# Kernel tuning notes

Measured on AMD Instinct MI355X. Metric: run time of the kernel, lower is better.

Reference implementation:

```python
import jax, jax.numpy as jnp
import numpy as np

NH = 12
LEVEL = 4  # Lmin = 2**LEVEL = 16


def _build_sets(T, Lmin):
    l_list, r_list = [], []
    L = Lmin
    while L <= T:
        for i in range(T // L):
            l_list.append(i * L)
            r_list.append((i + 1) * L - 1)
        L *= 2
    return np.asarray(l_list, np.int32), np.asarray(r_list, np.int32)


def _get_slice(x_cum, l_idx, r_idx):
    # x_cum: [B,nh,T,hs]; returns inclusive range-sums x[l..r] via cumsum diffs
    r = x_cum[:, :, r_idx, :]
    l = x_cum[:, :, np.maximum(np.asarray(l_idx) - 1, 0), :]
    mask = (np.asarray(l_idx) >= 1).astype(x_cum.dtype)[None, None, :, None]
    return r - l * mask


def _get_slice_dyn(x_cum, l_idx, r_idx):
    # same but with traced/jnp indices (tail term)
    r = x_cum[:, :, r_idx, :]
    l = x_cum[:, :, jnp.maximum(l_idx - 1, 0), :]
    mask = (l_idx >= 1).astype(x_cum.dtype)[None, None, :, None]
    return r - l * mask


def setup_inputs() -> dict:
    key = jax.random.key(0)
    k0, k1, k2, k3 = jax.random.split(key, 4)
    B, T, C = 8, 2048, 768
    hs = C // NH
    s = 0.02
    return {
        "x": jax.random.normal(k0, (B, T, C), jnp.float32),
        "Wqkv": jax.random.normal(k1, (3 * C, C), jnp.float32) * s,
        "Wproj": jax.random.normal(k2, (C, C), jnp.float32) * s,
        "Wv": jax.random.normal(k3, (hs, hs * hs), jnp.float32) * s,
        "bv": jnp.zeros((hs,), jnp.float32),
    }


def reference(x, Wqkv, Wproj, Wv, bv):
    B, T, C = x.shape
    nh = NH
    hs = C // nh
    Lmin = 2 ** LEVEL
    scale = 1.0 / jnp.sqrt(jnp.asarray(hs, x.dtype))

    qkv = x @ Wqkv.T  # [B,T,3C]
    q, k, v0 = jnp.split(qkv, 3, axis=-1)
    q = q.reshape(B, T, nh, hs).transpose(0, 2, 1, 3)   # [B,nh,T,hs]
    k = k.reshape(B, T, nh, hs).transpose(0, 2, 1, 3)
    v0 = v0.reshape(B, T, nh, hs).transpose(0, 2, 1, 3)

    # v = v_proj(outer(k, v0).flatten)  == einsum with Wv reshaped [hs,hs,hs]
    Wv3 = Wv.reshape(hs, hs, hs)
    v = jnp.einsum('bhti,bhtj,eij->bhte', k, v0, Wv3) + bv

    k_cum = jnp.cumsum(k, axis=2)
    v_cum = jnp.cumsum(v, axis=2)

    l_idx, r_idx = _build_sets(T, Lmin)  # static dyadic sets
    K = _get_slice(k_cum, l_idx, r_idx)  # [B,nh,S,hs]
    V = _get_slice(v_cum, l_idx, r_idx)

    t_idx = jnp.arange(T)
    mask = t_idx[:, None] >= jnp.asarray(r_idx)[None, :]  # [T,S]
    logits = jnp.einsum('bhtd,bhsd->bhts', q, K) * scale
    logits = jnp.where(mask[None, None], logits, -jnp.inf)

    # tail: remainder within the current Lmin block
    l_tail = (t_idx // Lmin) * Lmin
    K_tail = _get_slice_dyn(k_cum, l_tail, t_idx)  # [B,nh,T,hs]
    V_tail = _get_slice_dyn(v_cum, l_tail, t_idx)
    tail_logits = jnp.sum(q * K_tail, axis=-1) * scale  # [B,nh,T]

    att = jax.nn.softmax(jnp.concatenate([logits, tail_logits[..., None]], axis=-1), axis=-1)
    out = jnp.einsum('bhts,bhsd->bhtd', att[..., :-1], V) + att[..., -1:] * V_tail
    out = out.transpose(0, 2, 1, 3).reshape(B, T, C)
    return out @ Wproj.T
```

## Files before the change

kernel.cpp:

```cpp
#include <hip/hip_runtime.h>


typedef float  f32x4  __attribute__((ext_vector_type(4)));
typedef _Float16 half8 __attribute__((ext_vector_type(8)));
typedef _Float16 half4 __attribute__((ext_vector_type(4)));

#define DEV __device__ __forceinline__
#define MFMA16(a, b, c) __builtin_amdgcn_mfma_f32_16x16x32_f16((a), (b), (c), 0, 0, 0)
#define GLOAD16(gp, lp)                                                  \
  __builtin_amdgcn_global_load_lds(                                      \
      (const __attribute__((address_space(1))) unsigned int*)(gp),       \
      (__attribute__((address_space(3))) unsigned int*)(lp), 16, 0, 0)

__global__ __launch_bounds__(256) void k_cast16(const float* __restrict__ in,
                                                _Float16* __restrict__ outh, int n4) {
  int i = blockIdx.x * 256 + threadIdx.x;
  if (i >= n4) return;
  f32x4 v = ((const f32x4*)in)[i];
  half4 o;
#pragma unroll
  for (int c = 0; c < 4; ++c) o[c] = (_Float16)v[c];
  ((half4*)outh)[i] = o;
}

__global__ __launch_bounds__(256) void k_castw(const float* __restrict__ Wqkv,
                                               const float* __restrict__ Wv,
                                               const float* __restrict__ Wproj,
                                               _Float16* __restrict__ wq,
                                               _Float16* __restrict__ wv,
                                               _Float16* __restrict__ wp) {
  int i = blockIdx.x * 256 + threadIdx.x;
  const float* src;
  _Float16* dst;
  int idx = i;
  if (idx < 442368) { src = Wqkv; dst = wq; }
  else if (idx < 442368 + 65536) { src = Wv; dst = wv; idx -= 442368; }
  else if (idx < 442368 + 65536 + 147456) { src = Wproj; dst = wp; idx -= 442368 + 65536; }
  else return;
  f32x4 v = ((const f32x4*)src)[idx];
  half4 o;
#pragma unroll
  for (int c = 0; c < 4; ++c) o[c] = (_Float16)v[c];
  ((half4*)dst)[idx] = o;
}

__global__ __launch_bounds__(256, 3) void k_gemm_qkv(
    const _Float16* __restrict__ A16, const _Float16* __restrict__ B16,
    _Float16* __restrict__ qo, _Float16* __restrict__ ko, _Float16* __restrict__ v0o) {
  __shared__ _Float16 sA[128][64], sB[128][64];
  const int K = 768;
  int tid = threadIdx.x, lane = tid & 63, wave = tid >> 6;
  int l15 = lane & 15, g = lane >> 4;
  int wr = wave >> 1, wc = wave & 1;
  int wg = (blockIdx.x & 7) * 288 + (blockIdx.x >> 3);
  int n0 = (wg % 18) * 128, m0 = (wg / 18) * 128;
  f32x4 acc[4][4];
#pragma unroll
  for (int a = 0; a < 4; ++a)
#pragma unroll
    for (int b = 0; b < 4; ++b) acc[a][b] = f32x4{0.f, 0.f, 0.f, 0.f};
  int rsel = lane >> 3;
  int csel = (lane & 7) ^ rsel;
  for (int k0 = 0; k0 < K; k0 += 64) {
#pragma unroll
    for (int r = 0; r < 4; ++r) {
      int row = wave * 32 + r * 8 + rsel;
      GLOAD16(&A16[(size_t)(m0 + row) * K + k0 + csel * 8], &sA[wave * 32 + r * 8][0]);
      GLOAD16(&B16[(size_t)(n0 + row) * K + k0 + csel * 8], &sB[wave * 32 + r * 8][0]);
    }
    __syncthreads();
#pragma unroll
    for (int kk = 0; kk < 2; ++kk) {
      int kc = kk * 4 + g;
      int cc = ((kc ^ (l15 & 7)) << 3);
      half8 af[4], bf[4];
#pragma unroll
      for (int mf = 0; mf < 4; ++mf) af[mf] = *(const half8*)&sA[wr * 64 + mf * 16 + l15][cc];
#pragma unroll
      for (int nf = 0; nf < 4; ++nf) bf[nf] = *(const half8*)&sB[wc * 64 + nf * 16 + l15][cc];
#pragma unroll
      for (int mf = 0; mf < 4; ++mf)
#pragma unroll
        for (int nf = 0; nf < 4; ++nf)
          acc[mf][nf] = MFMA16(af[mf], bf[nf], acc[mf][nf]);
    }
    __syncthreads();
  }
  int sec = n0 / 768;
  int nb = n0 - sec * 768;
#pragma unroll
  for (int mf = 0; mf < 4; ++mf)
#pragma unroll
    for (int nf = 0; nf < 4; ++nf)
#pragma unroll
      for (int r = 0; r < 4; ++r) {
        int m = m0 + wr * 64 + mf * 16 + (g << 2) + r;
        int n = nb + wc * 64 + nf * 16 + l15;
        int b = m >> 11, t = m & 2047;
        int h = n >> 6, d = n & 63;
        size_t idx = (((size_t)b * 12 + h) * 2048 + t) * 64 + d;
        _Float16 val = (_Float16)acc[mf][nf][r];
        if (sec == 0) qo[idx] = val;
        else if (sec == 1) ko[idx] = val;
        else v0o[idx] = val;
      }
}

__global__ __launch_bounds__(256, 3) void k_veins(
    const _Float16* __restrict__ kh, const _Float16* __restrict__ v0g,
    const _Float16* __restrict__ Wvh, const float* __restrict__ bv,
    _Float16* __restrict__ vout) {
  __shared__ _Float16 ks[256][72];
  __shared__ _Float16 sB[2][64][64];
  int tid = threadIdx.x, lane = tid & 63, wave = tid >> 6;
  int l15 = lane & 15, g = lane >> 4, g8 = g << 3;
  size_t row0 = (size_t)blockIdx.x * 256;

  int srow_lo = wave * 8 + (lane >> 3);
  int scsrc = (lane & 7) ^ (lane >> 3);
  auto STAGE = [&](int b, int i) {
#pragma unroll
    for (int h = 0; h < 2; ++h) {
      GLOAD16(&Wvh[(size_t)(h * 32 + srow_lo) * 4096 + i * 64 + (scsrc << 3)],
              ((_Float16*)sB) + (size_t)b * 4096 + (h * 256 + wave * 64) * 8);
    }
  };

#pragma unroll
  for (int r = 0; r < 8; ++r) {
    int row = (tid >> 3) + r * 32;
    int c8 = (tid & 7) << 3;
    *(half8*)&ks[row][c8] = *(const half8*)&kh[(row0 + row) * 64 + c8];
  }
  half8 v0r[4][2];
#pragma unroll
  for (int mf = 0; mf < 4; ++mf) {
    size_t rb = (row0 + wave * 64 + mf * 16 + l15) * 64;
#pragma unroll
    for (int kk = 0; kk < 2; ++kk)
      v0r[mf][kk] = *(const half8*)&v0g[rb + kk * 32 + g8];
  }
  f32x4 acc[4][4];
#pragma unroll
  for (int a = 0; a < 4; ++a)
#pragma unroll
    for (int b = 0; b < 4; ++b) acc[a][b] = f32x4{0.f, 0.f, 0.f, 0.f};

  STAGE(0, 0);
  __syncthreads();
  int r0 = wave * 64 + l15;
  for (int i8 = 0; i8 < 8; ++i8) {
    half8 kr0 = *(const half8*)&ks[r0][i8 * 8];
    half8 kr1 = *(const half8*)&ks[r0 + 16][i8 * 8];
    half8 kr2 = *(const half8*)&ks[r0 + 32][i8 * 8];
    half8 kr3 = *(const half8*)&ks[r0 + 48][i8 * 8];
#pragma unroll
    for (int ii = 0; ii < 8; ++ii) {
      int i = i8 * 8 + ii;
      int cur = i & 1;
      if (i < 63) STAGE(cur ^ 1, i + 1);
      half8 b0[4], b1[4];
#pragma unroll
      for (int nf = 0; nf < 4; ++nf) {
        b0[nf] = *(const half8*)&sB[cur][nf * 16 + l15][((g ^ (l15 & 7)) << 3)];
        b1[nf] = *(const half8*)&sB[cur][nf * 16 + l15][(((4 + g) ^ (l15 & 7)) << 3)];
      }
      _Float16 kv0 = kr0[ii], kv1 = kr1[ii], kv2 = kr2[ii], kv3 = kr3[ii];
      {
        half8 a0 = v0r[0][0] * kv0, a1 = v0r[1][0] * kv1;
        half8 a2 = v0r[2][0] * kv2, a3 = v0r[3][0] * kv3;
#pragma unroll
        for (int nf = 0; nf < 4; ++nf) {
          acc[0][nf] = MFMA16(a0, b0[nf], acc[0][nf]);
          acc[1][nf] = MFMA16(a1, b0[nf], acc[1][nf]);
          acc[2][nf] = MFMA16(a2, b0[nf], acc[2][nf]);
          acc[3][nf] = MFMA16(a3, b0[nf], acc[3][nf]);
        }
      }
      {
        half8 a0 = v0r[0][1] * kv0, a1 = v0r[1][1] * kv1;
        half8 a2 = v0r[2][1] * kv2, a3 = v0r[3][1] * kv3;
#pragma unroll
        for (int nf = 0; nf < 4; ++nf) {
          acc[0][nf] = MFMA16(a0, b1[nf], acc[0][nf]);
          acc[1][nf] = MFMA16(a1, b1[nf], acc[1][nf]);
          acc[2][nf] = MFMA16(a2, b1[nf], acc[2][nf]);
          acc[3][nf] = MFMA16(a3, b1[nf], acc[3][nf]);
        }
      }
      __syncthreads();
    }
  }
#pragma unroll
  for (int mf = 0; mf < 4; ++mf)
#pragma unroll
    for (int nf = 0; nf < 4; ++nf) {
      int e = (nf << 4) + l15;
      float bve = bv[e];
#pragma unroll
      for (int r = 0; r < 4; ++r) {
        int row = wave * 64 + mf * 16 + (g << 2) + r;
        vout[(row0 + row) * 64 + e] = (_Float16)(acc[mf][nf][r] + bve);
      }
    }
}

__global__ __launch_bounds__(256) void k_segments(
    const _Float16* __restrict__ kmat, const _Float16* __restrict__ vmat,
    _Float16* __restrict__ Ks, _Float16* __restrict__ Vt) {
  __shared__ float Ls[255][64];
  int s = blockIdx.x;
  int bh = (s & 7) * 12 + (s >> 3);
  int tid = threadIdx.x;
  size_t bh2048 = (size_t)bh * 2048;
  for (int task = tid; task < 8192; task += 256) {
    int seg = task >> 6, d = task & 63;
    const _Float16* p = kmat + (bh2048 + seg * 16) * 64 + d;
    float sm = 0.f;
#pragma unroll
    for (int u = 0; u < 16; ++u) sm += (float)p[u * 64];
    Ls[seg][d] = sm;
  }
  __syncthreads();
  {
    int bprev = 0, bcur = 128, cnt = 64;
    for (int lev = 1; lev < 8; ++lev) {
      for (int task = tid; task < cnt * 64; task += 256) {
        int i = task >> 6, d = task & 63;
        Ls[bcur + i][d] = Ls[bprev + 2 * i][d] + Ls[bprev + 2 * i + 1][d];
      }
      __syncthreads();
      bprev = bcur; bcur += cnt; cnt >>= 1;
    }
  }
  for (int task = tid; task < 16384; task += 256) {
    int seg = task >> 6;
    float v = (seg < 255) ? Ls[seg][task & 63] : 0.f;
    Ks[(size_t)bh * 16384 + task] = (_Float16)v;
  }
  __syncthreads();
  for (int task = tid; task < 8192; task += 256) {
    int seg = task >> 6, d = task & 63;
    const _Float16* p = vmat + (bh2048 + seg * 16) * 64 + d;
    float sm = 0.f;
#pragma unroll
    for (int u = 0; u < 16; ++u) sm += (float)p[u * 64];
    Ls[seg][d] = sm;
  }
  __syncthreads();
  {
    int bprev = 0, bcur = 128, cnt = 64;
    for (int lev = 1; lev < 8; ++lev) {
      for (int task = tid; task < cnt * 64; task += 256) {
        int i = task >> 6, d = task & 63;
        Ls[bcur + i][d] = Ls[bprev + 2 * i][d] + Ls[bprev + 2 * i + 1][d];
      }
      __syncthreads();
      bprev = bcur; bcur += cnt; cnt >>= 1;
    }
  }
  for (int task = tid; task < 16384; task += 256) {
    int d = task >> 8, seg = task & 255;
    float v = (seg < 255) ? Ls[seg][d] : 0.f;
    Vt[(size_t)bh * 16384 + task] = (_Float16)v;
  }
}

__global__ __launch_bounds__(256) void k_tails(
    const _Float16* __restrict__ km, const _Float16* __restrict__ vm,
    _Float16* __restrict__ tKg, _Float16* __restrict__ tVt) {
  int B = blockIdx.x;
  int bh = (B & 7) * 12 + (B >> 6);
  int seg16 = ((B >> 3) & 7) * 16;
  int wave = threadIdx.x >> 6, lane = threadIdx.x & 63;
  for (int task = wave; task < 32; task += 4) {
    int blk = seg16 + (task >> 1);
    size_t base = ((size_t)bh * 2048 + blk * 16) * 64 + lane;
    if (!(task & 1)) {
      float ka = 0.f;
      _Float16* o = tKg + (((size_t)bh * 128 + blk) * 16) * 64 + lane;
#pragma unroll
      for (int t = 0; t < 16; ++t) {
        ka += (float)km[base + t * 64];
        o[t * 64] = (_Float16)ka;
      }
    } else {
      float va = 0.f;
      half8 lo = {}, hi = {};
#pragma unroll
      for (int t = 0; t < 8; ++t) {
        va += (float)vm[base + t * 64];
        lo[t] = (_Float16)va;
      }
#pragma unroll
      for (int t = 0; t < 8; ++t) {
        va += (float)vm[base + (t + 8) * 64];
        hi[t] = (_Float16)va;
      }
      _Float16* o = tVt + (((size_t)bh * 128 + blk) * 64 + lane) * 16;
      ((half8*)o)[0] = lo;
      ((half8*)o)[1] = hi;
    }
  }
}

__global__ __launch_bounds__(256, 3) void k_attn2(
    const _Float16* __restrict__ qm,
    const _Float16* __restrict__ tKg, const _Float16* __restrict__ tVt,
    const _Float16* __restrict__ Ks, const _Float16* __restrict__ Vt,
    _Float16* __restrict__ outp) {
  __shared__ __align__(16) _Float16 P[4][16][280];
  __shared__ __align__(16) _Float16 sKs[2][32][64];
  __shared__ __align__(16) _Float16 sVt[2][64][32];
  int tid = threadIdx.x, lane = tid & 63, wave = tid >> 6;
  int orig = blockIdx.y * 32 + blockIdx.x;
  int wg = (orig & 7) * 384 + (orig >> 3);
  int tile = wg & 31, bh = wg >> 5;
  int t0 = tile * 64, tw0 = t0 + wave * 16;
  int blkw = tile * 4 + wave;
  size_t bh2048 = (size_t)bh * 2048;
  int l15 = lane & 15, g = lane >> 4, g8 = g << 3;

  const _Float16* KsB = Ks + (size_t)bh * 16384;
  const _Float16* VB = Vt + (size_t)bh * 16384;

  auto STAGE_K = [&](int buf, int c) {
    GLOAD16(KsB + (size_t)(c * 32 + wave * 8 + (lane >> 3)) * 64 +
                (((lane & 7) ^ ((lane >> 3) & 7)) << 3),
            &sKs[buf][wave * 8][0]);
  };
  auto STAGE_VT = [&](int buf, int c) {
    GLOAD16(VB + (size_t)(wave * 16 + (lane >> 2)) * 256 + c * 32 +
                (((lane & 3) ^ ((lane >> 2) & 3)) << 3),
            &sVt[buf][wave * 16][0]);
  };

  half8 qf0, qf1, t0f, t1f;
  {
    const _Float16* qp = qm + (bh2048 + tw0 + l15) * 64 + g8;
    qf0 = *(const half8*)qp;
    qf1 = *(const half8*)(qp + 32);
    const _Float16* tp = tKg + (((size_t)bh * 128 + blkw) * 16 + l15) * 64 + g8;
    t0f = *(const half8*)tp;
    t1f = *(const half8*)(tp + 32);
  }
  STAGE_K(0, 0);

  unsigned mA = 0, mE = 0;
#pragma unroll
  for (int nf = 0; nf < 16; ++nf) {
    int seg = nf * 16 + l15;
    if (seg < 255) {
      int m = 256 - seg;
      int cl = 32 - __clz(m - 1);
      int lev = 8 - cl;
      int rdx = (seg - (256 - (256 >> lev)) + 1) * (16 << lev) - 1;
      if (rdx < tw0) mA |= 1u << nf;
      else if (rdx == tw0 + 15) mE |= 1u << nf;
    }
  }

  f32x4 acc[17];
#pragma unroll
  for (int i = 0; i < 17; ++i) acc[i] = f32x4{0.f, 0.f, 0.f, 0.f};

  __syncthreads();
#pragma unroll
  for (int c = 0; c < 8; ++c) {
    if (c < 7) STAGE_K((c + 1) & 1, c + 1);
    int bs = c & 1;
#pragma unroll
    for (int p = 0; p < 2; ++p) {
      int row = p * 16 + l15;
      half8 b0 = *(const half8*)&sKs[bs][row][(g ^ (l15 & 7)) << 3];
      half8 b1 = *(const half8*)&sKs[bs][row][((g + 4) ^ (l15 & 7)) << 3];
      acc[2 * c + p] = MFMA16(qf0, b0, acc[2 * c + p]);
      acc[2 * c + p] = MFMA16(qf1, b1, acc[2 * c + p]);
    }
    __syncthreads();
  }
  acc[16] = MFMA16(qf0, t0f, acc[16]);
  acc[16] = MFMA16(qf1, t1f, acc[16]);

  STAGE_VT(0, 0);
  STAGE_VT(1, 1);

  const float c2 = 0.125f * 1.44269504f;
  float mx[4], sm[4], et[4];
#pragma unroll
  for (int r = 0; r < 4; ++r) {
    int tr = g * 4 + r;
    mx[r] = (l15 == tr) ? acc[16][r] * c2 : -3.0e38f;
  }
#pragma unroll
  for (int nf = 0; nf < 16; ++nf) {
    bool bA = (mA >> nf) & 1, bE = (mE >> nf) & 1;
#pragma unroll
    for (int r = 0; r < 4; ++r) {
      bool u = bA || (bE && g == 3 && r == 3);
      if (u) mx[r] = fmaxf(mx[r], acc[nf][r] * c2);
    }
  }
#pragma unroll
  for (int off = 1; off < 16; off <<= 1)
#pragma unroll
    for (int r = 0; r < 4; ++r) mx[r] = fmaxf(mx[r], __shfl_xor(mx[r], off));
#pragma unroll
  for (int r = 0; r < 4; ++r) {
    int tr = g * 4 + r;
    et[r] = (l15 == tr) ? exp2f(acc[16][r] * c2 - mx[r]) : 0.f;
    sm[r] = et[r];
  }
#pragma unroll
  for (int nf = 0; nf < 16; ++nf) {
    bool bA = (mA >> nf) & 1, bE = (mE >> nf) & 1;
#pragma unroll
    for (int r = 0; r < 4; ++r) {
      bool u = bA || (bE && g == 3 && r == 3);
      float e = u ? exp2f(acc[nf][r] * c2 - mx[r]) : 0.f;
      acc[nf][r] = e;
      sm[r] += e;
    }
  }
#pragma unroll
  for (int off = 1; off < 16; off <<= 1)
#pragma unroll
    for (int r = 0; r < 4; ++r) sm[r] += __shfl_xor(sm[r], off);
  float inv[4];
#pragma unroll
  for (int r = 0; r < 4; ++r) inv[r] = 1.f / sm[r];

  {
    half4 z4 = {};
    *(half4*)&P[wave][lane >> 2][256 + (lane & 3) * 4] = z4;
  }
#pragma unroll
  for (int nf = 0; nf < 16; ++nf)
#pragma unroll
    for (int r = 0; r < 4; ++r)
      P[wave][g * 4 + r][nf * 16 + l15] = (_Float16)acc[nf][r];
#pragma unroll
  for (int r = 0; r < 4; ++r)
    if (l15 == g * 4 + r) P[wave][l15][256 + l15] = (_Float16)et[r];

  f32x4 oa[4];
#pragma unroll
  for (int i = 0; i < 4; ++i) oa[i] = f32x4{0.f, 0.f, 0.f, 0.f};
  __syncthreads();
#pragma unroll
  for (int c = 0; c < 8; ++c) {
    int bs = c & 1;
    half8 pa = *(const half8*)&P[wave][l15][c * 32 + g8];
#pragma unroll
    for (int n2 = 0; n2 < 4; ++n2) {
      half8 vb = *(const half8*)&sVt[bs][n2 * 16 + l15][(g ^ (l15 & 3)) << 3];
      oa[n2] = MFMA16(pa, vb, oa[n2]);
    }
    __syncthreads();
    if (c < 6) STAGE_VT(bs, c + 2);
  }
  {
    half8 pa = *(const half8*)&P[wave][l15][256 + (g & 1) * 8];
    const _Float16* tvb = tVt + ((size_t)bh * 128 + blkw) * 1024;
#pragma unroll
    for (int n2 = 0; n2 < 4; ++n2) {
      half8 vt = {};
      if (g < 2)
        vt = *(const half8*)(tvb + (size_t)(n2 * 16 + l15) * 16 + g8);
      oa[n2] = MFMA16(pa, vt, oa[n2]);
    }
  }
  int b = bh / 12, h = bh - b * 12;
  size_t obase = ((size_t)b * 2048 + tw0) * 768 + h * 64;
#pragma unroll
  for (int n2 = 0; n2 < 4; ++n2)
#pragma unroll
    for (int r = 0; r < 4; ++r)
      outp[obase + (size_t)(g * 4 + r) * 768 + n2 * 16 + l15] = (_Float16)(oa[n2][r] * inv[r]);
}

__global__ __launch_bounds__(256, 3) void k_gemm_proj(
    const _Float16* __restrict__ A16, const _Float16* __restrict__ B16,
    float* __restrict__ C) {
  __shared__ _Float16 sA[128][64], sB[128][64];
  const int K = 768;
  int tid = threadIdx.x, lane = tid & 63, wave = tid >> 6;
  int l15 = lane & 15, g = lane >> 4;
  int wr = wave >> 1, wc = wave & 1;
  int wg = (blockIdx.x & 7) * 96 + (blockIdx.x >> 3);
  int n0 = (wg % 6) * 128, m0 = (wg / 6) * 128;
  f32x4 acc[4][4];
#pragma unroll
  for (int a = 0; a < 4; ++a)
#pragma unroll
    for (int b = 0; b < 4; ++b) acc[a][b] = f32x4{0.f, 0.f, 0.f, 0.f};
  int rsel = lane >> 3;
  int csel = (lane & 7) ^ rsel;
  for (int k0 = 0; k0 < K; k0 += 64) {
#pragma unroll
    for (int r = 0; r < 4; ++r) {
      int row = wave * 32 + r * 8 + rsel;
      GLOAD16(&A16[(size_t)(m0 + row) * K + k0 + csel * 8], &sA[wave * 32 + r * 8][0]);
      GLOAD16(&B16[(size_t)(n0 + row) * K + k0 + csel * 8], &sB[wave * 32 + r * 8][0]);
    }
    __syncthreads();
#pragma unroll
    for (int kk = 0; kk < 2; ++kk) {
      int kc = kk * 4 + g;
      int cc = ((kc ^ (l15 & 7)) << 3);
      half8 af[4], bf[4];
#pragma unroll
      for (int mf = 0; mf < 4; ++mf) af[mf] = *(const half8*)&sA[wr * 64 + mf * 16 + l15][cc];
#pragma unroll
      for (int nf = 0; nf < 4; ++nf) bf[nf] = *(const half8*)&sB[wc * 64 + nf * 16 + l15][cc];
#pragma unroll
      for (int mf = 0; mf < 4; ++mf)
#pragma unroll
        for (int nf = 0; nf < 4; ++nf)
          acc[mf][nf] = MFMA16(af[mf], bf[nf], acc[mf][nf]);
    }
    __syncthreads();
  }
#pragma unroll
  for (int mf = 0; mf < 4; ++mf)
#pragma unroll
    for (int nf = 0; nf < 4; ++nf)
#pragma unroll
      for (int r = 0; r < 4; ++r) {
        int m = m0 + wr * 64 + mf * 16 + (g << 2) + r;
        int n = n0 + wc * 64 + nf * 16 + l15;
        C[(size_t)m * 768 + n] = acc[mf][nf][r];
      }
}

extern "C" void kernel_launch(void* const* d_in, const int* in_sizes, int n_in,
                              void* d_out, int out_size, void* d_ws, size_t ws_size,
                              hipStream_t stream) {
  const float* x = (const float*)d_in[0];
  const float* Wqkv = (const float*)d_in[1];
  const float* Wproj = (const float*)d_in[2];
  const float* Wv = (const float*)d_in[3];
  const float* bv = (const float*)d_in[4];
  float* out = (float*)d_out;
  char* ws = (char*)d_ws;
  size_t off = 0;
  auto alloc = [&](size_t bytes) -> void* {
    void* p = (void*)(ws + off);
    off += (bytes + 255) & ~(size_t)255;
    return p;
  };
  _Float16* x16  = (_Float16*)alloc(12582912ull * 2);
  _Float16* wq16 = (_Float16*)alloc(1769472ull * 2);
  _Float16* wv16 = (_Float16*)alloc(262144ull * 2 + 8192);
  _Float16* wp16 = (_Float16*)alloc(589824ull * 2);
  _Float16* q16  = (_Float16*)alloc(12582912ull * 2);
  _Float16* k16  = (_Float16*)alloc(12582912ull * 2);
  _Float16* v016 = (_Float16*)alloc(12582912ull * 2);
  _Float16* vm16 = (_Float16*)alloc(12582912ull * 2);
  _Float16* Ks   = (_Float16*)alloc(1572864ull * 2);
  _Float16* Vt   = (_Float16*)alloc(1572864ull * 2);
  _Float16* tKg  = (_Float16*)alloc(12582912ull * 2);
  _Float16* tVt  = (_Float16*)alloc(12582912ull * 2);
  _Float16* outp = (_Float16*)alloc(12582912ull * 2);

  k_cast16<<<dim3(12288), dim3(256), 0, stream>>>(x, x16, 3145728);
  k_castw<<<dim3(2560), dim3(256), 0, stream>>>(Wqkv, Wv, Wproj, wq16, wv16, wp16);
  k_gemm_qkv<<<dim3(2304), dim3(256), 0, stream>>>(x16, wq16, q16, k16, v016);
  k_veins<<<dim3(768), dim3(256), 0, stream>>>(k16, v016, wv16, bv, vm16);
  k_segments<<<dim3(96), dim3(256), 0, stream>>>(k16, vm16, Ks, Vt);
  k_tails<<<dim3(768), dim3(256), 0, stream>>>(k16, vm16, tKg, tVt);
  k_attn2<<<dim3(32, 96), dim3(256), 0, stream>>>(q16, tKg, tVt, Ks, Vt, outp);
  k_gemm_proj<<<dim3(768), dim3(256), 0, stream>>>(outp, wp16, out);
}
```

Baseline: 307.4 us.

## Reuse tail block sums for segment hierarchy and merge cast kernels

The tails kernel now also writes each 16-token block's full K and V sums in fp32. A new lightweight hierarchy kernel builds the dyadic segment sums from those block sums, so the 96-block segments kernel no longer re-reads all of k and v. The two cast kernels are merged into one launch. This trades a second pass over k16/vm16 by a low-parallelism kernel for extra small fp32 buffers and one fewer launch.

```diff
diff --git a/kernel.cpp b/kernel.cpp
--- a/kernel.cpp
+++ b/kernel.cpp
@@ -12,30 +12,19 @@
       (const __attribute__((address_space(1))) unsigned int*)(gp),       \
       (__attribute__((address_space(3))) unsigned int*)(lp), 16, 0, 0)
 
-__global__ __launch_bounds__(256) void k_cast16(const float* __restrict__ in,
-                                                _Float16* __restrict__ outh, int n4) {
-  int i = blockIdx.x * 256 + threadIdx.x;
-  if (i >= n4) return;
-  f32x4 v = ((const f32x4*)in)[i];
-  half4 o;
-#pragma unroll
-  for (int c = 0; c < 4; ++c) o[c] = (_Float16)v[c];
-  ((half4*)outh)[i] = o;
-}
-
-__global__ __launch_bounds__(256) void k_castw(const float* __restrict__ Wqkv,
-                                               const float* __restrict__ Wv,
-                                               const float* __restrict__ Wproj,
-                                               _Float16* __restrict__ wq,
-                                               _Float16* __restrict__ wv,
-                                               _Float16* __restrict__ wp) {
+__global__ __launch_bounds__(256) void k_castall(
+    const float* __restrict__ x, const float* __restrict__ Wqkv,
+    const float* __restrict__ Wv, const float* __restrict__ Wproj,
+    _Float16* __restrict__ x16, _Float16* __restrict__ wq,
+    _Float16* __restrict__ wv, _Float16* __restrict__ wp) {
   int i = blockIdx.x * 256 + threadIdx.x;
   const float* src;
   _Float16* dst;
   int idx = i;
-  if (idx < 442368) { src = Wqkv; dst = wq; }
-  else if (idx < 442368 + 65536) { src = Wv; dst = wv; idx -= 442368; }
-  else if (idx < 442368 + 65536 + 147456) { src = Wproj; dst = wp; idx -= 442368 + 65536; }
+  if (idx < 3145728) { src = x; dst = x16; }
+  else if (idx < 3145728 + 442368) { src = Wqkv; dst = wq; idx -= 3145728; }
+  else if (idx < 3145728 + 442368 + 65536) { src = Wv; dst = wv; idx -= 3145728 + 442368; }
+  else if (idx < 3145728 + 442368 + 65536 + 147456) { src = Wproj; dst = wp; idx -= 3145728 + 442368 + 65536; }
   else return;
   f32x4 v = ((const f32x4*)src)[idx];
   half4 o;
@@ -205,70 +194,10 @@
     }
 }
 
-__global__ __launch_bounds__(256) void k_segments(
-    const _Float16* __restrict__ kmat, const _Float16* __restrict__ vmat,
-    _Float16* __restrict__ Ks, _Float16* __restrict__ Vt) {
-  __shared__ float Ls[255][64];
-  int s = blockIdx.x;
-  int bh = (s & 7) * 12 + (s >> 3);
-  int tid = threadIdx.x;
-  size_t bh2048 = (size_t)bh * 2048;
-  for (int task = tid; task < 8192; task += 256) {
-    int seg = task >> 6, d = task & 63;
-    const _Float16* p = kmat + (bh2048 + seg * 16) * 64 + d;
-    float sm = 0.f;
-#pragma unroll
-    for (int u = 0; u < 16; ++u) sm += (float)p[u * 64];
-    Ls[seg][d] = sm;
-  }
-  __syncthreads();
-  {
-    int bprev = 0, bcur = 128, cnt = 64;
-    for (int lev = 1; lev < 8; ++lev) {
-      for (int task = tid; task < cnt * 64; task += 256) {
-        int i = task >> 6, d = task & 63;
-        Ls[bcur + i][d] = Ls[bprev + 2 * i][d] + Ls[bprev + 2 * i + 1][d];
-      }
-      __syncthreads();
-      bprev = bcur; bcur += cnt; cnt >>= 1;
-    }
-  }
-  for (int task = tid; task < 16384; task += 256) {
-    int seg = task >> 6;
-    float v = (seg < 255) ? Ls[seg][task & 63] : 0.f;
-    Ks[(size_t)bh * 16384 + task] = (_Float16)v;
-  }
-  __syncthreads();
-  for (int task = tid; task < 8192; task += 256) {
-    int seg = task >> 6, d = task & 63;
-    const _Float16* p = vmat + (bh2048 + seg * 16) * 64 + d;
-    float sm = 0.f;
-#pragma unroll
-    for (int u = 0; u < 16; ++u) sm += (float)p[u * 64];
-    Ls[seg][d] = sm;
-  }
-  __syncthreads();
-  {
-    int bprev = 0, bcur = 128, cnt = 64;
-    for (int lev = 1; lev < 8; ++lev) {
-      for (int task = tid; task < cnt * 64; task += 256) {
-        int i = task >> 6, d = task & 63;
-        Ls[bcur + i][d] = Ls[bprev + 2 * i][d] + Ls[bprev + 2 * i + 1][d];
-      }
-      __syncthreads();
-      bprev = bcur; bcur += cnt; cnt >>= 1;
-    }
-  }
-  for (int task = tid; task < 16384; task += 256) {
-    int d = task >> 8, seg = task & 255;
-    float v = (seg < 255) ? Ls[seg][d] : 0.f;
-    Vt[(size_t)bh * 16384 + task] = (_Float16)v;
-  }
-}
-
 __global__ __launch_bounds__(256) void k_tails(
     const _Float16* __restrict__ km, const _Float16* __restrict__ vm,
-    _Float16* __restrict__ tKg, _Float16* __restrict__ tVt) {
+    _Float16* __restrict__ tKg, _Float16* __restrict__ tVt,
+    float* __restrict__ L0K, float* __restrict__ L0V) {
   int B = blockIdx.x;
   int bh = (B & 7) * 12 + (B >> 6);
   int seg16 = ((B >> 3) & 7) * 16;
@@ -284,6 +213,7 @@
         ka += (float)km[base + t * 64];
         o[t * 64] = (_Float16)ka;
       }
+      L0K[((size_t)bh * 128 + blk) * 64 + lane] = ka;
     } else {
       float va = 0.f;
       half8 lo = {}, hi = {};
@@ -300,7 +230,56 @@
       _Float16* o = tVt + (((size_t)bh * 128 + blk) * 64 + lane) * 16;
       ((half8*)o)[0] = lo;
       ((half8*)o)[1] = hi;
-    }
+      L0V[((size_t)bh * 128 + blk) * 64 + lane] = va;
+    }
+  }
+}
+
+__global__ __launch_bounds__(256) void k_hier(
+    const float* __restrict__ L0K, const float* __restrict__ L0V,
+    _Float16* __restrict__ Ks, _Float16* __restrict__ Vt) {
+  __shared__ float Ls[255][64];
+  int s = blockIdx.x;
+  int bh = (s & 7) * 12 + (s >> 3);
+  int tid = threadIdx.x;
+  for (int task = tid; task < 8192; task += 256)
+    Ls[task >> 6][task & 63] = L0K[(size_t)bh * 8192 + task];
+  __syncthreads();
+  {
+    int bprev = 0, bcur = 128, cnt = 64;
+    for (int lev = 1; lev < 8; ++lev) {
+      for (int task = tid; task < cnt * 64; task += 256) {
+        int i = task >> 6, d = task & 63;
+        Ls[bcur + i][d] = Ls[bprev + 2 * i][d] + Ls[bprev + 2 * i + 1][d];
+      }
+      __syncthreads();
+      bprev = bcur; bcur += cnt; cnt >>= 1;
+    }
+  }
+  for (int task = tid; task < 16384; task += 256) {
+    int seg = task >> 6;
+    float v = (seg < 255) ? Ls[seg][task & 63] : 0.f;
+    Ks[(size_t)bh * 16384 + task] = (_Float16)v;
+  }
+  __syncthreads();
+  for (int task = tid; task < 8192; task += 256)
+    Ls[task >> 6][task & 63] = L0V[(size_t)bh * 8192 + task];
+  __syncthreads();
+  {
+    int bprev = 0, bcur = 128, cnt = 64;
+    for (int lev = 1; lev < 8; ++lev) {
+      for (int task = tid; task < cnt * 64; task += 256) {
+        int i = task >> 6, d = task & 63;
+        Ls[bcur + i][d] = Ls[bprev + 2 * i][d] + Ls[bprev + 2 * i + 1][d];
+      }
+      __syncthreads();
+      bprev = bcur; bcur += cnt; cnt >>= 1;
+    }
+  }
+  for (int task = tid; task < 16384; task += 256) {
+    int d = task >> 8, seg = task & 255;
+    float v = (seg < 255) ? Ls[seg][d] : 0.f;
+    Vt[(size_t)bh * 16384 + task] = (_Float16)v;
   }
 }
 
@@ -561,14 +540,15 @@
   _Float16* Vt   = (_Float16*)alloc(1572864ull * 2);
   _Float16* tKg  = (_Float16*)alloc(12582912ull * 2);
   _Float16* tVt  = (_Float16*)alloc(12582912ull * 2);
+  float*    L0K  = (float*)alloc(786432ull * 4);
+  float*    L0V  = (float*)alloc(786432ull * 4);
   _Float16* outp = (_Float16*)alloc(12582912ull * 2);
 
-  k_cast16<<<dim3(12288), dim3(256), 0, stream>>>(x, x16, 3145728);
-  k_castw<<<dim3(2560), dim3(256), 0, stream>>>(Wqkv, Wv, Wproj, wq16, wv16, wp16);
+  k_castall<<<dim3(14848), dim3(256), 0, stream>>>(x, Wqkv, Wv, Wproj, x16, wq16, wv16, wp16);
   k_gemm_qkv<<<dim3(2304), dim3(256), 0, stream>>>(x16, wq16, q16, k16, v016);
   k_veins<<<dim3(768), dim3(256), 0, stream>>>(k16, v016, wv16, bv, vm16);
-  k_segments<<<dim3(96), dim3(256), 0, stream>>>(k16, vm16, Ks, Vt);
-  k_tails<<<dim3(768), dim3(256), 0, stream>>>(k16, vm16, tKg, tVt);
+  k_tails<<<dim3(768), dim3(256), 0, stream>>>(k16, vm16, tKg, tVt, L0K, L0V);
+  k_hier<<<dim3(96), dim3(256), 0, stream>>>(L0K, L0V, Ks, Vt);
   k_attn2<<<dim3(32, 96), dim3(256), 0, stream>>>(q16, tKg, tVt, Ks, Vt, outp);
   k_gemm_proj<<<dim3(768), dim3(256), 0, stream>>>(outp, wp16, out);
 }
```

Measured after the change: 292.7 us (median of 2 runs). -4.8%, faster.
